# Kernel tuning notes

Measured on AMD Instinct MI355X. Metric: run time of the kernel, lower is better.

The kernel has to match this reference:

```python
import jax, jax.numpy as jnp
import numpy as np

S = 128           # inp_spatial_size
B = 4             # batch (4th coord column)
N = 200000        # active voxels
PLANES = (4, 8, 16, 32)   # feat_aug_mode='power', m=4
LEAK = 0.01
EPS = 1e-4        # sparseconvnet BatchNorm default eps
NOUT = 64


def _conv(x, w, stride, pad):
    return jax.lax.conv_general_dilated(
        x, w, (stride,) * 3, pad,
        dimension_numbers=('NCDHW', 'OIDHW', 'NCDHW'))


def _bn_lrelu(x, mask, g, b):
    # SCN BatchNormLeakyReLU: stats over ACTIVE sites only (x is zero at inactive)
    cnt = jnp.maximum(jnp.sum(mask), 1.0)
    mean = jnp.sum(x, axis=(0, 2, 3, 4)) / cnt
    var = jnp.sum(x * x, axis=(0, 2, 3, 4)) / cnt - mean * mean
    sc = (g * jax.lax.rsqrt(var + EPS))[None, :, None, None, None]
    y = (x - mean[None, :, None, None, None]) * sc + b[None, :, None, None, None]
    y = jnp.where(y >= 0, y, LEAK * y)
    return y * mask


def _pool2(x, red):
    b, c, d, h, w = x.shape
    return red(x.reshape(b, c, d // 2, 2, h // 2, 2, w // 2, 2), axis=(3, 5, 7))


def _forward(point_cloud, w0, g1, b1, wc1, g2, b2, wc2, g3, b3, wc3, wlin, blin):
    ci = point_cloud[:, :3].astype(jnp.int32)
    bi = point_cloud[:, 3].astype(jnp.int32)
    f = point_cloud[:, 4]
    # InputLayer mode=3: sum features of duplicate coordinates
    dense = jnp.zeros((B, 1, S, S, S), jnp.float32).at[bi, 0, ci[:, 0], ci[:, 1], ci[:, 2]].add(f)
    mask = jnp.zeros((B, 1, S, S, S), jnp.float32).at[bi, 0, ci[:, 0], ci[:, 1], ci[:, 2]].set(1.0)
    # SubmanifoldConvolution(3): dense 3^3 conv restricted to active output sites
    x = _conv(dense, w0, 1, 'SAME') * mask
    for g, b, wc in ((g1, b1, wc1), (g2, b2, wc2), (g3, b3, wc3)):
        x = _bn_lrelu(x, mask, g, b)
        x = _conv(x, wc, 2, 'VALID')        # sparse Convolution(k=2, s=2)
        mask = _pool2(mask, jnp.max)        # output active iff any input in window active
        x = x * mask
        x = _pool2(x, jnp.sum) / 8.0        # SCN AveragePooling(2,2): sum / poolVolume
        mask = _pool2(mask, jnp.max)
        x = x * mask
    # SparseToDense(32) + view(-1, D^3*C): row-major [B, C, D, D, D] flatten
    x = x.reshape(x.shape[0], -1)           # [B, 32*2^3] = [B, 256]
    return x @ wlin.T + blin                # use_linear_output -> [B, 64]


def setup_inputs() -> dict:
    key = jax.random.key(0)
    ks = jax.random.split(key, 10)
    coords = jax.random.randint(ks[0], (N, 3), 0, S).astype(jnp.float32)
    bidx = jax.random.randint(ks[1], (N, 1), 0, B).astype(jnp.float32)
    feats = jax.random.normal(ks[2], (N, 1), jnp.float32)
    point_cloud = jnp.concatenate([coords, bidx, feats], axis=1)

    def he(k, shape, fan_in):
        return jax.random.normal(k, shape, jnp.float32) / np.sqrt(fan_in)

    inp = {
        'point_cloud': point_cloud,
        'w0': he(ks[3], (PLANES[0], 1, 3, 3, 3), 27.0),
    }
    for i in range(3):
        cin, cout = PLANES[i], PLANES[i + 1]
        inp[f'g{i + 1}'] = jnp.ones((cin,), jnp.float32)
        inp[f'b{i + 1}'] = jnp.zeros((cin,), jnp.float32)
        inp[f'wc{i + 1}'] = he(ks[4 + i], (cout, cin, 2, 2, 2), cin * 8.0)
    d = S // 4 ** 3
    fan = PLANES[-1] * d ** 3
    inp['wlin'] = he(ks[8], (NOUT, fan), fan)
    inp['blin'] = jnp.zeros((NOUT,), jnp.float32)
    return inp


def reference(point_cloud, w0, g1, b1, wc1, g2, b2, wc2, g3, b3, wc3, wlin, blin):
    return _forward(point_cloud, w0, g1, b1, wc1, g2, b2, wc2, g3, b3, wc3, wlin, blin)
```

## Files before the change

kernel.cpp:

```cpp
#include <hip/hip_runtime.h>

#define SS 128
#define S3 (SS*SS*SS)
#define NBATCH 4
#define LEAK 0.01f
#define BNEPS 1e-4f
#define NTILE 16384
#define MAXSLOT 64

constexpr size_t OFF_DENSE    = 0;
constexpr size_t OFF_MASKBITS = OFF_DENSE + (size_t)NBATCH*S3*4;
constexpr size_t OFF_X1       = OFF_MASKBITS + (size_t)NBATCH*S3/8;
constexpr size_t OFF_MASK32   = OFF_X1 + (size_t)NBATCH*8*32768*4;
constexpr size_t OFF_MASK8    = OFF_MASK32 + (size_t)NBATCH*32768;
constexpr size_t OFF_STATS    = OFF_MASK8 + (size_t)NBATCH*512;
constexpr size_t OFF_P1       = OFF_STATS + 256;
constexpr size_t OFF_P2       = OFF_P1 + 256*9*4;
constexpr size_t OFF_P3       = OFF_P2 + 256*2*4;
constexpr size_t OFF_PM       = OFF_P3 + 64*2*4;
constexpr size_t OFF_NBLK     = OFF_PM + 16*4;
constexpr size_t OFF_LIST     = OFF_NBLK + NTILE*4;
constexpr size_t OFF_X0L      = OFF_LIST + (size_t)NTILE*MAXSLOT*4;
constexpr size_t OFF_X2       = OFF_X0L + (size_t)NTILE*MAXSLOT*16;
constexpr size_t OFF_X3       = OFF_X2 + (size_t)NBATCH*16*512*4;


__device__ inline float waveSum(float v) {
#pragma unroll
    for (int off = 32; off; off >>= 1) v += __shfl_xor(v, off, 64);
    return v;
}

__global__ void k_init(const float* __restrict__ pc, float* __restrict__ dense,
                       uint4* __restrict__ maskbits4, int n) {
    int blk = blockIdx.x;
    if (blk < 256) {
        maskbits4[blk * 256 + threadIdx.x] = make_uint4(0u, 0u, 0u, 0u);
        return;
    }
    int i = (blk - 256) * 256 + threadIdx.x;
    if (i >= n) return;
    int d = (int)pc[i*5+0], h = (int)pc[i*5+1], w = (int)pc[i*5+2], b = (int)pc[i*5+3];
    dense[(((size_t)b*SS + d)*SS + h)*SS + w] = 0.f;
}

__global__ void k_scatter(const float* __restrict__ pc, float* __restrict__ dense,
                          unsigned* __restrict__ maskbits, int n) {
    int i = blockIdx.x * blockDim.x + threadIdx.x;
    if (i >= n) return;
    float c0 = pc[i*5+0], c1 = pc[i*5+1], c2 = pc[i*5+2], cb = pc[i*5+3], f = pc[i*5+4];
    int d = (int)c0, h = (int)c1, w = (int)c2, b = (int)cb;
    unsigned vox = (((unsigned)b*SS + d)*SS + h)*SS + w;
    atomicAdd(&dense[vox], f);
    atomicOr(&maskbits[vox >> 5], 1u << (vox & 31));
}

__global__ __launch_bounds__(512) void k_conv0(const float* __restrict__ dense,
                                               const unsigned* __restrict__ maskbits,
                                               const float* __restrict__ w0g,
                                               unsigned* __restrict__ nblk,
                                               unsigned* __restrict__ list,
                                               float4* __restrict__ x0l,
                                               unsigned char* __restrict__ mask32) {
    __shared__ float lds[10*10*68];
    __shared__ float ws[108];
    __shared__ unsigned short wtot[8][8];
    __shared__ unsigned queue[8*MAXSLOT];
    __shared__ unsigned char cellocc[8][8];
    int tid = threadIdx.x;
    int lane = tid & 63, wid = tid >> 6;
    int th = blockIdx.x, td = blockIdx.y;
    int zb = blockIdx.z;
    int b = zb >> 1, wh = zb & 1;
    int d0 = td*8, h0 = th*8, w0 = wh*64;
    if (tid < 108) ws[tid] = w0g[tid];
    if (tid < 64) cellocc[tid>>3][tid&7] = 0;
    const float* dn = dense + (size_t)b * S3;
    for (int idx = tid; idx < 1600; idx += 512) {
        int r = idx >> 4, q = idx & 15;
        int dz = r / 10, dy = r - dz*10;
        int gz = d0 - 1 + dz, gy = h0 - 1 + dy;
        float4 v = make_float4(0.f, 0.f, 0.f, 0.f);
        if ((unsigned)gz < SS && (unsigned)gy < SS) {
            unsigned row = ((unsigned)b*SS + gz)*SS + gy;
            int gx = w0 + q*4;
            v = *(const float4*)(dn + ((size_t)gz*SS + gy)*SS + gx);
            unsigned mword = maskbits[row*4 + (gx >> 5)];
            int sh = gx & 31;
            if (!((mword >> (sh+0)) & 1u)) v.x = 0.f;
            if (!((mword >> (sh+1)) & 1u)) v.y = 0.f;
            if (!((mword >> (sh+2)) & 1u)) v.z = 0.f;
            if (!((mword >> (sh+3)) & 1u)) v.w = 0.f;
        }
        float* lrow = lds + r*68 + 1 + q*4;
        lrow[0]=v.x; lrow[1]=v.y; lrow[2]=v.z; lrow[3]=v.w;
    }
    for (int idx = tid; idx < 200; idx += 512) {
        int r = idx >> 1, side = idx & 1;
        int dz = r / 10, dy = r - dz*10;
        int gz = d0 - 1 + dz, gy = h0 - 1 + dy;
        int hgx = side ? (w0 + 64) : (w0 - 1);
        float hv = 0.f;
        if ((unsigned)gz < SS && (unsigned)gy < SS && (unsigned)hgx < SS) {
            unsigned row = ((unsigned)b*SS + gz)*SS + gy;
            float v = dn[((size_t)gz*SS + gy)*SS + hgx];
            unsigned mword = maskbits[row*4 + (hgx >> 5)];
            hv = ((mword >> (hgx & 31)) & 1u) ? v : 0.f;
        }
        lds[r*68 + (side ? 65 : 0)] = hv;
    }
    int tz = wid, ty = (tid >> 3) & 7, tx = tid & 7;
    int gz = d0 + tz, gy = h0 + ty;
    uint4 rb = ((const uint4*)maskbits)[((unsigned)b*SS + gz)*SS + gy];
    unsigned loW = wh ? rb.z : rb.x;
    unsigned hiW = wh ? rb.w : rb.y;
    unsigned occ8 = 0;
#pragma unroll
    for (int s=0;s<8;++s) {
        unsigned word = (s < 4) ? loW : hiW;
        occ8 |= (((word >> (((s&3)<<3) + tx)) & 1u) << s);
    }
    unsigned long long ballArr[8];
#pragma unroll
    for (int s=0;s<8;++s) {
        ballArr[s] = __ballot((occ8 >> s) & 1u);
        if (lane == 0) wtot[s][wid] = (unsigned short)__popcll(ballArr[s]);
    }
    __syncthreads();
    unsigned long long lmask = (1ull << lane) - 1ull;
    int blkbase = ((b*16 + td)*16 + th)*16 + wh*8;
    unsigned qb = 0;
#pragma unroll
    for (int s=0;s<8;++s) {
        unsigned base = 0, total = 0;
#pragma unroll
        for (int j=0;j<8;++j) { unsigned t = wtot[s][j]; if (j < wid) base += t; total += t; }
        unsigned tc = total < MAXSLOT ? total : MAXSLOT;
        if ((occ8 >> s) & 1u) {
            unsigned slot = base + (unsigned)__popcll(ballArr[s] & lmask);
            if (slot < MAXSLOT) queue[qb + slot] = (unsigned)tid | (s<<9) | (slot<<13);
            cellocc[s][((tz>>2)<<2) | ((ty>>2)<<1) | (tx>>2)] = 1;
        }
        qb += tc;
    }
    if (tid < 8) {
        unsigned total = 0;
#pragma unroll
        for (int j=0;j<8;++j) total += wtot[tid][j];
        nblk[blkbase + tid] = total < MAXSLOT ? total : MAXSLOT;
    }
    __syncthreads();
    if (tid < 64) {
        int s = tid >> 3, c = tid & 7;
        int cz = (c>>2)&1, cy = (c>>1)&1, cx = c&1;
        mask32[b*32768 + ((d0>>2)+cz)*1024 + ((h0>>2)+cy)*32 + wh*16 + s*2+cx] = cellocc[s][c];
    }
    for (unsigned i = tid; i < qb; i += 512) {
        unsigned e = queue[i];
        int et = e & 511, es = (e>>9) & 15, eslot = e >> 13;
        int ez = et >> 6, ey = (et>>3) & 7, ex = et & 7;
        int egx = es*8 + ex;
        float a0=0.f, a1=0.f, a2=0.f, a3=0.f;
#pragma unroll
        for (int kd=0; kd<3; ++kd)
#pragma unroll
            for (int kh=0; kh<3; ++kh)
#pragma unroll
                for (int kw=0; kw<3; ++kw) {
                    float v = lds[((ez+kd)*10 + ey+kh)*68 + egx + kw];
                    int kk = kd*9 + kh*3 + kw;
                    a0 += v*ws[kk]; a1 += v*ws[27+kk]; a2 += v*ws[54+kk]; a3 += v*ws[81+kk];
                }
        int blk = blkbase + es;
        unsigned vox = (((unsigned)b*SS + d0+ez)*SS + h0+ey)*SS + (w0 + egx);
        list[(size_t)blk*MAXSLOT + eslot] = vox;
        x0l[(size_t)blk*MAXSLOT + eslot] = make_float4(a0, a1, a2, a3);
    }
}

__global__ void k_stats1m(const float4* __restrict__ x0l, const unsigned* __restrict__ nblk,
                          const unsigned char* __restrict__ mask32, unsigned char* __restrict__ mask8,
                          float* __restrict__ p1, float* __restrict__ pm) {
    int tid = threadIdx.x;
    int bid = blockIdx.x;
    if (bid < 256) {
        __shared__ float red[4][9];
        int tid0 = bid * 256 + tid;
        float a[9] = {0,0,0,0,0,0,0,0,0};
        for (int s = tid0; s < NTILE*MAXSLOT; s += 65536) {
            int blk = s >> 6, sl = s & 63;
            if (sl < (int)nblk[blk]) {
                float4 v = x0l[s];
                a[0]+=v.x; a[1]+=v.y; a[2]+=v.z; a[3]+=v.w;
                a[4]+=v.x*v.x; a[5]+=v.y*v.y; a[6]+=v.z*v.z; a[7]+=v.w*v.w;
                a[8]+=1.f;
            }
        }
#pragma unroll
        for (int k=0;k<9;++k) a[k] = waveSum(a[k]);
        int wid = tid>>6, lane = tid&63;
        if (lane < 9) red[wid][lane] = a[lane];
        __syncthreads();
        if (tid < 9) p1[bid*9+tid] = red[0][tid]+red[1][tid]+red[2][tid]+red[3][tid];
        return;
    }
    __shared__ float redm[4];
    int blk = bid - 256;
    float c = 0.f;
    if (blk < 8) {
        int i = blk*256 + tid;
        int b = i>>9, r = i&511;
        int d8 = r>>6, h8 = (r>>3)&7, w8 = r&7;
        const unsigned char* m = mask32 + b*32768;
        unsigned v = 0;
#pragma unroll
        for (int dz=0;dz<2;++dz)
#pragma unroll
            for (int dy=0;dy<2;++dy)
#pragma unroll
                for (int dx=0;dx<2;++dx)
                    v |= m[(2*d8+dz)*1024 + (2*h8+dy)*32 + (2*w8+dx)];
        mask8[i] = (unsigned char)v;
        c = (float)v;
    } else {
        const uint4* m4 = (const uint4*)mask32;
        int base = ((blk-8)*256 + tid)*4;
#pragma unroll
        for (int j=0;j<4;++j) {
            uint4 x = m4[base+j];
            c += (float)(__popc(x.x) + __popc(x.y) + __popc(x.z) + __popc(x.w));
        }
    }
    c = waveSum(c);
    if ((tid & 63) == 0) redm[tid>>6] = c;
    __syncthreads();
    if (tid == 0) pm[blk] = redm[0]+redm[1]+redm[2]+redm[3];
}

__global__ __launch_bounds__(256) void k_prep1(const float* __restrict__ p1,
        const float* __restrict__ pm, const float* __restrict__ g1,
        const float* __restrict__ b1, float* __restrict__ stats) {
    __shared__ float red[4][9];
    __shared__ float tot[9];
    int tid = threadIdx.x;
    int wid = tid>>6, lane = tid&63;
    float a[9];
#pragma unroll
    for (int k=0;k<9;++k) a[k] = p1[tid*9+k];
#pragma unroll
    for (int k=0;k<9;++k) a[k] = waveSum(a[k]);
    if (lane < 9) red[wid][lane] = a[lane];
    __syncthreads();
    if (tid < 9) tot[tid] = red[0][tid]+red[1][tid]+red[2][tid]+red[3][tid];
    __syncthreads();
    if (tid < 4) {
        float cnt = fmaxf(tot[8], 1.f);
        float mean = tot[tid] / cnt;
        float var  = tot[4+tid] / cnt - mean*mean;
        float s = g1[tid] * rsqrtf(var + BNEPS);
        stats[2+tid] = s; stats[6+tid] = b1[tid] - mean*s;
    }
    if (tid == 4) { float s=0.f; for (int j=8;j<16;++j) s += pm[j]; stats[0] = s; }
    if (tid == 5) { float s=0.f; for (int j=0;j<8;++j)  s += pm[j]; stats[1] = s; }
}

__global__ void k_stage1(const float4* __restrict__ x0l, const unsigned* __restrict__ list,
                         const unsigned* __restrict__ nblk, const float* __restrict__ wc1,
                         const float* __restrict__ stats, float* __restrict__ x1) {
    __shared__ float acc[256];
    __shared__ float wsh[256];
    __shared__ float sc[4], sh[4];
    int tid = threadIdx.x;
    wsh[tid] = wc1[tid];
    acc[tid] = 0.f;
    if (tid < 4) { sc[tid] = stats[2+tid]; sh[tid] = stats[6+tid]; }
    __syncthreads();
    int s = blockIdx.x * 256 + tid;
    int blk = s >> 6, sl = s & 63;
    int lt = tid >> 6;
    if (sl < (int)nblk[blk]) {
        unsigned vox = list[s];
        float4 v = x0l[s];
        int w = vox & 127, h = (vox>>7)&127, d = (vox>>14)&127;
        float y[4];
        float t0 = v.x*sc[0]+sh[0]; y[0] = t0 >= 0.f ? t0 : LEAK*t0;
        float t1 = v.y*sc[1]+sh[1]; y[1] = t1 >= 0.f ? t1 : LEAK*t1;
        float t2 = v.z*sc[2]+sh[2]; y[2] = t2 >= 0.f ? t2 : LEAK*t2;
        float t3 = v.w*sc[3]+sh[3]; y[3] = t3 >= 0.f ? t3 : LEAK*t3;
        int widx = (d&1)*4 + (h&1)*2 + (w&1);
        int cell = ((d>>2)&1)*4 + ((h>>2)&1)*2 + ((w>>2)&1);
        float* ap = acc + lt*64 + cell;
#pragma unroll
        for (int o=0;o<8;++o) {
            const float* wp = wsh + o*32 + widx;
            float contrib = y[0]*wp[0] + y[1]*wp[8] + y[2]*wp[16] + y[3]*wp[24];
            atomicAdd(ap + o*8, contrib * 0.125f);
        }
    }
    __syncthreads();
    int rem = tid & 63, o = rem >> 3, cell = rem & 7;
    int blk2 = blockIdx.x*4 + (tid >> 6);
    int ss = blk2 & 15, th = (blk2>>4)&15, td = (blk2>>8)&15, b = blk2>>12;
    int cz = (cell>>2)&1, cy = (cell>>1)&1, cx = cell&1;
    x1[(size_t)b*8*32768 + o*32768 + (td*2+cz)*1024 + (th*2+cy)*32 + ss*2+cx] = acc[tid];
}

__global__ void k_s2stats(const float4* __restrict__ x1v, float* __restrict__ p2) {
    __shared__ float red[4][2];
    int blk = blockIdx.x;
    int plane = blk >> 3, chunk = blk & 7;
    const float4* p = x1v + (size_t)plane*8192 + chunk*1024;
    float s=0.f, sq=0.f;
    for (int i = threadIdx.x; i < 1024; i += 256) {
        float4 v = p[i];
        s  += v.x+v.y+v.z+v.w;
        sq += v.x*v.x+v.y*v.y+v.z*v.z+v.w*v.w;
    }
    s = waveSum(s); sq = waveSum(sq);
    int wid = threadIdx.x>>6, lane = threadIdx.x&63;
    if (lane == 0) { red[wid][0] = s; red[wid][1] = sq; }
    __syncthreads();
    if (threadIdx.x < 2)
        p2[blk*2+threadIdx.x] = red[0][threadIdx.x]+red[1][threadIdx.x]+red[2][threadIdx.x]+red[3][threadIdx.x];
}

__global__ void k_prep2(const float* __restrict__ p2, const float* __restrict__ g2,
                        const float* __restrict__ b2, float* __restrict__ stats) {
    __shared__ float sm[16];
    int tid = threadIdx.x;
    if (tid < 16) {
        int c = tid & 7, q = tid >> 3;
        float s = 0.f;
        for (int b=0;b<4;++b)
            for (int ch=0;ch<8;++ch)
                s += p2[((b*8+c)*8+ch)*2 + q];
        sm[tid] = s;
    }
    __syncthreads();
    if (tid < 8) {
        float cnt = fmaxf(stats[0], 1.f);
        float mean = sm[tid] / cnt;
        float var  = sm[8+tid] / cnt - mean*mean;
        float s = g2[tid] * rsqrtf(var + BNEPS);
        stats[10+tid] = s; stats[18+tid] = b2[tid] - mean*s;
    }
}

__global__ __launch_bounds__(256) void k_stage2(const float* __restrict__ x1,
                         const unsigned char* __restrict__ mask32,
                         const float* __restrict__ wc2, const float* __restrict__ stats,
                         float* __restrict__ x2) {
    __shared__ float wsh[1024];
    __shared__ float xin[8][64];
    __shared__ float mLDS[64];
    __shared__ float scs[8], shs[8];
    int tid = threadIdx.x;
    int br = blockIdx.x;
    int b = br >> 9, r = br & 511;
    int d8 = r >> 6, h8 = (r >> 3) & 7, w8 = r & 7;
    for (int i = tid; i < 1024; i += 256) wsh[i] = wc2[i];
    if (tid < 8) { scs[tid] = stats[10+tid]; shs[tid] = stats[18+tid]; }
    const unsigned char* mb = mask32 + b*32768;
    if (tid < 64) {
        int dd = tid >> 4, hh = (tid >> 2) & 3, ww = tid & 3;
        mLDS[tid] = mb[(d8*4+dd)*1024 + (h8*4+hh)*32 + (w8*4+ww)] ? 1.f : 0.f;
    }
    __syncthreads();
    if (tid < 128) {
        int c = tid >> 4, f = tid & 15;
        int dd = f >> 2, hh = f & 3;
        const float* src = x1 + (size_t)b*8*32768 + c*32768
                         + (d8*4+dd)*1024 + (h8*4+hh)*32 + w8*4;
        float4 v = *(const float4*)src;
        float sc = scs[c], sh = shs[c];
        int cbase = dd*16 + hh*4;
        float t0 = v.x*sc+sh; t0 = (t0>=0.f)?t0:LEAK*t0; xin[c][cbase+0] = t0 * mLDS[cbase+0];
        float t1 = v.y*sc+sh; t1 = (t1>=0.f)?t1:LEAK*t1; xin[c][cbase+1] = t1 * mLDS[cbase+1];
        float t2 = v.z*sc+sh; t2 = (t2>=0.f)?t2:LEAK*t2; xin[c][cbase+2] = t2 * mLDS[cbase+2];
        float t3 = v.w*sc+sh; t3 = (t3>=0.f)?t3:LEAK*t3; xin[c][cbase+3] = t3 * mLDS[cbase+3];
    }
    __syncthreads();
    int o = tid >> 4, g = tid & 15;
    float acc = 0.f;
#pragma unroll
    for (int j=0;j<4;++j) {
        int cell = g*4 + j;
        int dd = cell >> 4, hh = (cell >> 2) & 3, ww = cell & 3;
        int widx = (dd&1)*4 + (hh&1)*2 + (ww&1);
        const float* wp = wsh + o*64 + widx;
#pragma unroll
        for (int c=0;c<8;++c)
            acc += xin[c][cell] * wp[c*8];
    }
    acc += __shfl_xor(acc, 1, 64);
    acc += __shfl_xor(acc, 2, 64);
    acc += __shfl_xor(acc, 4, 64);
    acc += __shfl_xor(acc, 8, 64);
    if (g == 0) x2[((size_t)b*16 + o)*512 + r] = acc * 0.125f;
}

__global__ void k_s3stats(const float* __restrict__ x2, float* __restrict__ p3) {
    __shared__ float red[4][2];
    const float* p = x2 + (size_t)blockIdx.x * 512;
    float s=0.f, sq=0.f;
    for (int i = threadIdx.x; i < 512; i += 256) { float v = p[i]; s += v; sq += v*v; }
    s = waveSum(s); sq = waveSum(sq);
    int wid = threadIdx.x>>6, lane = threadIdx.x&63;
    if (lane == 0) { red[wid][0] = s; red[wid][1] = sq; }
    __syncthreads();
    if (threadIdx.x < 2)
        p3[blockIdx.x*2+threadIdx.x] = red[0][threadIdx.x]+red[1][threadIdx.x]+red[2][threadIdx.x]+red[3][threadIdx.x];
}

__global__ void k_prep3(const float* __restrict__ p3, const float* __restrict__ g3,
                        const float* __restrict__ b3, float* __restrict__ stats) {
    __shared__ float sm[32];
    int tid = threadIdx.x;
    if (tid < 32) {
        int c = tid & 15, q = tid >> 4;
        float s = 0.f;
        for (int b=0;b<4;++b) s += p3[(b*16+c)*2 + q];
        sm[tid] = s;
    }
    __syncthreads();
    if (tid < 16) {
        float cnt = fmaxf(stats[1], 1.f);
        float mean = sm[tid] / cnt;
        float var  = sm[16+tid] / cnt - mean*mean;
        float s = g3[tid] * rsqrtf(var + BNEPS);
        stats[26+tid] = s; stats[42+tid] = b3[tid] - mean*s;
    }
}

__global__ void k_stage3(const float* __restrict__ x2, const unsigned char* __restrict__ mask8,
                         const float* __restrict__ wc3, const float* __restrict__ stats,
                         float* __restrict__ x3) {
    int t = blockIdx.x * 4 + (threadIdx.x >> 6);
    int lane = threadIdx.x & 63;
    int r = t & 7, bo = t >> 3;
    int o = bo & 31, b = bo >> 5;
    int d2 = (r >> 2) & 1, h2 = (r >> 1) & 1, w2 = r & 1;
    int dd = lane >> 4, hh = (lane >> 2) & 3, ww = lane & 3;
    int s8 = (d2*4+dd)*64 + (h2*4+hh)*8 + (w2*4+ww);
    const float* xb = x2 + (size_t)b*16*512;
    float w0r = wc3[o*128 + lane];
    float w1r = wc3[o*128 + 64 + lane];
    float m = mask8[b*512 + s8] ? 1.f : 0.f;
    int widx = (dd&1)*4 + (hh&1)*2 + (ww&1);
    float acc = 0.f;
#pragma unroll
    for (int c=0;c<8;++c) {
        float v = xb[c*512 + s8];
        float tt = v*stats[26+c] + stats[42+c];
        tt = (tt >= 0.f) ? tt : LEAK*tt;
        acc += tt * __shfl(w0r, c*8 + widx, 64);
    }
#pragma unroll
    for (int c=8;c<16;++c) {
        float v = xb[c*512 + s8];
        float tt = v*stats[26+c] + stats[42+c];
        tt = (tt >= 0.f) ? tt : LEAK*tt;
        acc += tt * __shfl(w1r, (c-8)*8 + widx, 64);
    }
    acc = waveSum(acc * m);
    if (lane == 0) x3[t] = acc * 0.125f;
}

__global__ void k_linear(const float* __restrict__ x3, const float* __restrict__ wlin,
                         const float* __restrict__ blin, float* __restrict__ out) {
    int t = blockIdx.x * 4 + (threadIdx.x >> 6);
    int lane = threadIdx.x & 63;
    int b = t >> 6, j = t & 63;
    const float* xb = x3 + b*256;
    const float* wj = wlin + j*256;
    float acc = 0.f;
#pragma unroll
    for (int k=0;k<4;++k) acc += xb[k*64+lane] * wj[k*64+lane];
    acc = waveSum(acc);
    if (lane == 0) out[t] = acc + blin[j];
}

extern "C" void kernel_launch(void* const* d_in, const int* in_sizes, int n_in,
                              void* d_out, int out_size, void* d_ws, size_t ws_size,
                              hipStream_t stream) {
    const float* pc   = (const float*)d_in[0];
    const float* w0   = (const float*)d_in[1];
    const float* g1   = (const float*)d_in[2];
    const float* b1   = (const float*)d_in[3];
    const float* wc1  = (const float*)d_in[4];
    const float* g2   = (const float*)d_in[5];
    const float* b2   = (const float*)d_in[6];
    const float* wc2  = (const float*)d_in[7];
    const float* g3   = (const float*)d_in[8];
    const float* b3   = (const float*)d_in[9];
    const float* wc3  = (const float*)d_in[10];
    const float* wlin = (const float*)d_in[11];
    const float* blin = (const float*)d_in[12];
    float* out = (float*)d_out;

    char* ws = (char*)d_ws;
    float*         dense    = (float*)(ws + OFF_DENSE);
    unsigned*      maskbits = (unsigned*)(ws + OFF_MASKBITS);
    float*         x1       = (float*)(ws + OFF_X1);
    unsigned char* mask32   = (unsigned char*)(ws + OFF_MASK32);
    unsigned char* mask8    = (unsigned char*)(ws + OFF_MASK8);
    float*         stats    = (float*)(ws + OFF_STATS);
    float*         p1       = (float*)(ws + OFF_P1);
    float*         p2       = (float*)(ws + OFF_P2);
    float*         p3       = (float*)(ws + OFF_P3);
    float*         pm       = (float*)(ws + OFF_PM);
    unsigned*      nblk     = (unsigned*)(ws + OFF_NBLK);
    unsigned*      list     = (unsigned*)(ws + OFF_LIST);
    float4*        x0l      = (float4*)(ws + OFF_X0L);
    float*         x2       = (float*)(ws + OFF_X2);
    float*         x3       = (float*)(ws + OFF_X3);

    int n = in_sizes[0] / 5;
    int nb = (n + 255) / 256;

    k_init<<<256 + nb, 256, 0, stream>>>(pc, dense, (uint4*)maskbits, n);
    k_scatter<<<nb, 256, 0, stream>>>(pc, dense, maskbits, n);
    k_conv0<<<dim3(16,16,8), 512, 0, stream>>>(dense, maskbits, w0, nblk, list, x0l, mask32);
    k_stats1m<<<272, 256, 0, stream>>>(x0l, nblk, mask32, mask8, p1, pm);
    k_prep1<<<1, 256, 0, stream>>>(p1, pm, g1, b1, stats);
    k_stage1<<<NTILE/4, 256, 0, stream>>>(x0l, list, nblk, wc1, stats, x1);
    k_s2stats<<<256, 256, 0, stream>>>((const float4*)x1, p2);
    k_prep2<<<1, 64, 0, stream>>>(p2, g2, b2, stats);
    k_stage2<<<2048, 256, 0, stream>>>(x1, mask32, wc2, stats, x2);
    k_s3stats<<<64, 256, 0, stream>>>(x2, p3);
    k_prep3<<<1, 64, 0, stream>>>(p3, g3, b3, stats);
    k_stage3<<<256, 256, 0, stream>>>(x2, mask8, wc3, stats, x3);
    k_linear<<<64, 256, 0, stream>>>(x3, wlin, blin, out);
}
```

Before: 100.4 us.

## Fold BN prep kernels into stage kernels and gather only active voxels in conv0

Removes the three single-block BN statistics kernels (prep1/2/3): each stage kernel now reduces the partial sums and computes its own scale and shift in shared memory, which cuts three launches and the serialization they add. Separately, the conv0 tile load now zero-fills LDS and reads only the voxels whose mask bit is set, instead of loading full float4 rows and masking them. The cost is redundant per-block reduction work in every stage block, and a divergent bit-loop gather in place of coalesced vector loads.

```diff
diff --git a/kernel.cpp b/kernel.cpp
--- a/kernel.cpp
+++ b/kernel.cpp
@@ -13,8 +13,7 @@
 constexpr size_t OFF_X1       = OFF_MASKBITS + (size_t)NBATCH*S3/8;
 constexpr size_t OFF_MASK32   = OFF_X1 + (size_t)NBATCH*8*32768*4;
 constexpr size_t OFF_MASK8    = OFF_MASK32 + (size_t)NBATCH*32768;
-constexpr size_t OFF_STATS    = OFF_MASK8 + (size_t)NBATCH*512;
-constexpr size_t OFF_P1       = OFF_STATS + 256;
+constexpr size_t OFF_P1       = OFF_MASK8 + (size_t)NBATCH*512;
 constexpr size_t OFF_P2       = OFF_P1 + 256*9*4;
 constexpr size_t OFF_P3       = OFF_P2 + 256*2*4;
 constexpr size_t OFF_PM       = OFF_P3 + 64*2*4;
@@ -23,7 +22,6 @@
 constexpr size_t OFF_X0L      = OFF_LIST + (size_t)NTILE*MAXSLOT*4;
 constexpr size_t OFF_X2       = OFF_X0L + (size_t)NTILE*MAXSLOT*16;
 constexpr size_t OFF_X3       = OFF_X2 + (size_t)NBATCH*16*512*4;
-
 
 __device__ inline float waveSum(float v) {
 #pragma unroll
@@ -62,7 +60,7 @@
                                                unsigned* __restrict__ list,
                                                float4* __restrict__ x0l,
                                                unsigned char* __restrict__ mask32) {
-    __shared__ float lds[10*10*68];
+    __shared__ __align__(16) float lds[10*10*68];
     __shared__ float ws[108];
     __shared__ unsigned short wtot[8][8];
     __shared__ unsigned queue[8*MAXSLOT];
@@ -75,39 +73,36 @@
     int d0 = td*8, h0 = th*8, w0 = wh*64;
     if (tid < 108) ws[tid] = w0g[tid];
     if (tid < 64) cellocc[tid>>3][tid&7] = 0;
+    for (int i = tid; i < 1700; i += 512) ((float4*)lds)[i] = make_float4(0.f,0.f,0.f,0.f);
+    __syncthreads();
     const float* dn = dense + (size_t)b * S3;
-    for (int idx = tid; idx < 1600; idx += 512) {
-        int r = idx >> 4, q = idx & 15;
+    for (int idx = tid; idx < 200; idx += 512) {
+        int r = idx >> 1, ww2 = idx & 1;
         int dz = r / 10, dy = r - dz*10;
         int gz = d0 - 1 + dz, gy = h0 - 1 + dy;
-        float4 v = make_float4(0.f, 0.f, 0.f, 0.f);
-        if ((unsigned)gz < SS && (unsigned)gy < SS) {
-            unsigned row = ((unsigned)b*SS + gz)*SS + gy;
-            int gx = w0 + q*4;
-            v = *(const float4*)(dn + ((size_t)gz*SS + gy)*SS + gx);
-            unsigned mword = maskbits[row*4 + (gx >> 5)];
-            int sh = gx & 31;
-            if (!((mword >> (sh+0)) & 1u)) v.x = 0.f;
-            if (!((mword >> (sh+1)) & 1u)) v.y = 0.f;
-            if (!((mword >> (sh+2)) & 1u)) v.z = 0.f;
-            if (!((mword >> (sh+3)) & 1u)) v.w = 0.f;
+        if ((unsigned)gz >= SS || (unsigned)gy >= SS) continue;
+        const float* rowp = dn + ((size_t)gz*SS + gy)*SS;
+        unsigned rowi = ((unsigned)b*SS + gz)*SS + gy;
+        unsigned m = maskbits[rowi*4 + wh*2 + ww2];
+        float* lrow = lds + r*68 + 1 + ww2*32;
+        int gbase = w0 + ww2*32;
+        while (m) {
+            int bit = __ffs(m) - 1; m &= m - 1;
+            lrow[bit] = rowp[gbase + bit];
         }
-        float* lrow = lds + r*68 + 1 + q*4;
-        lrow[0]=v.x; lrow[1]=v.y; lrow[2]=v.z; lrow[3]=v.w;
-    }
-    for (int idx = tid; idx < 200; idx += 512) {
-        int r = idx >> 1, side = idx & 1;
-        int dz = r / 10, dy = r - dz*10;
-        int gz = d0 - 1 + dz, gy = h0 - 1 + dy;
-        int hgx = side ? (w0 + 64) : (w0 - 1);
-        float hv = 0.f;
-        if ((unsigned)gz < SS && (unsigned)gy < SS && (unsigned)hgx < SS) {
-            unsigned row = ((unsigned)b*SS + gz)*SS + gy;
-            float v = dn[((size_t)gz*SS + gy)*SS + hgx];
-            unsigned mword = maskbits[row*4 + (hgx >> 5)];
-            hv = ((mword >> (hgx & 31)) & 1u) ? v : 0.f;
+        if (ww2 == 0) {
+            int hgx = w0 - 1;
+            if (hgx >= 0) {
+                unsigned hm = maskbits[rowi*4 + (hgx>>5)];
+                if ((hm >> (hgx&31)) & 1u) lds[r*68] = rowp[hgx];
+            }
+        } else {
+            int hgx = w0 + 64;
+            if (hgx < SS) {
+                unsigned hm = maskbits[rowi*4 + (hgx>>5)];
+                if ((hm >> (hgx&31)) & 1u) lds[r*68 + 65] = rowp[hgx];
+            }
         }
-        lds[r*68 + (side ? 65 : 0)] = hv;
     }
     int tz = wid, ty = (tid >> 3) & 7, tx = tid & 7;
     int gz = d0 + tz, gy = h0 + ty;
@@ -237,13 +232,18 @@
     if (tid == 0) pm[blk] = redm[0]+redm[1]+redm[2]+redm[3];
 }
 
-__global__ __launch_bounds__(256) void k_prep1(const float* __restrict__ p1,
-        const float* __restrict__ pm, const float* __restrict__ g1,
-        const float* __restrict__ b1, float* __restrict__ stats) {
+__global__ void k_stage1(const float4* __restrict__ x0l, const unsigned* __restrict__ list,
+                         const unsigned* __restrict__ nblk, const float* __restrict__ wc1,
+                         const float* __restrict__ p1, const float* __restrict__ g1,
+                         const float* __restrict__ b1, float* __restrict__ x1) {
+    __shared__ float acc[256];
+    __shared__ float wsh[256];
     __shared__ float red[4][9];
-    __shared__ float tot[9];
+    __shared__ float sc[4], sh[4];
     int tid = threadIdx.x;
     int wid = tid>>6, lane = tid&63;
+    wsh[tid] = wc1[tid];
+    acc[tid] = 0.f;
     float a[9];
 #pragma unroll
     for (int k=0;k<9;++k) a[k] = p1[tid*9+k];
@@ -251,29 +251,14 @@
     for (int k=0;k<9;++k) a[k] = waveSum(a[k]);
     if (lane < 9) red[wid][lane] = a[lane];
     __syncthreads();
-    if (tid < 9) tot[tid] = red[0][tid]+red[1][tid]+red[2][tid]+red[3][tid];
-    __syncthreads();
     if (tid < 4) {
-        float cnt = fmaxf(tot[8], 1.f);
-        float mean = tot[tid] / cnt;
-        float var  = tot[4+tid] / cnt - mean*mean;
+        float sum = red[0][tid]+red[1][tid]+red[2][tid]+red[3][tid];
+        float sq  = red[0][4+tid]+red[1][4+tid]+red[2][4+tid]+red[3][4+tid];
+        float cnt = fmaxf(red[0][8]+red[1][8]+red[2][8]+red[3][8], 1.f);
+        float mean = sum/cnt, var = sq/cnt - mean*mean;
         float s = g1[tid] * rsqrtf(var + BNEPS);
-        stats[2+tid] = s; stats[6+tid] = b1[tid] - mean*s;
-    }
-    if (tid == 4) { float s=0.f; for (int j=8;j<16;++j) s += pm[j]; stats[0] = s; }
-    if (tid == 5) { float s=0.f; for (int j=0;j<8;++j)  s += pm[j]; stats[1] = s; }
-}
-
-__global__ void k_stage1(const float4* __restrict__ x0l, const unsigned* __restrict__ list,
-                         const unsigned* __restrict__ nblk, const float* __restrict__ wc1,
-                         const float* __restrict__ stats, float* __restrict__ x1) {
-    __shared__ float acc[256];
-    __shared__ float wsh[256];
-    __shared__ float sc[4], sh[4];
-    int tid = threadIdx.x;
-    wsh[tid] = wc1[tid];
-    acc[tid] = 0.f;
-    if (tid < 4) { sc[tid] = stats[2+tid]; sh[tid] = stats[6+tid]; }
+        sc[tid] = s; sh[tid] = b1[tid] - mean*s;
+    }
     __syncthreads();
     int s = blockIdx.x * 256 + tid;
     int blk = s >> 6, sl = s & 63;
@@ -324,46 +309,43 @@
         p2[blk*2+threadIdx.x] = red[0][threadIdx.x]+red[1][threadIdx.x]+red[2][threadIdx.x]+red[3][threadIdx.x];
 }
 
-__global__ void k_prep2(const float* __restrict__ p2, const float* __restrict__ g2,
-                        const float* __restrict__ b2, float* __restrict__ stats) {
-    __shared__ float sm[16];
-    int tid = threadIdx.x;
-    if (tid < 16) {
-        int c = tid & 7, q = tid >> 3;
-        float s = 0.f;
-        for (int b=0;b<4;++b)
-            for (int ch=0;ch<8;++ch)
-                s += p2[((b*8+c)*8+ch)*2 + q];
-        sm[tid] = s;
-    }
-    __syncthreads();
-    if (tid < 8) {
-        float cnt = fmaxf(stats[0], 1.f);
-        float mean = sm[tid] / cnt;
-        float var  = sm[8+tid] / cnt - mean*mean;
-        float s = g2[tid] * rsqrtf(var + BNEPS);
-        stats[10+tid] = s; stats[18+tid] = b2[tid] - mean*s;
-    }
-}
-
 __global__ __launch_bounds__(256) void k_stage2(const float* __restrict__ x1,
                          const unsigned char* __restrict__ mask32,
-                         const float* __restrict__ wc2, const float* __restrict__ stats,
-                         float* __restrict__ x2) {
+                         const float* __restrict__ wc2, const float* __restrict__ p2,
+                         const float* __restrict__ pm, const float* __restrict__ g2,
+                         const float* __restrict__ b2, float* __restrict__ x2) {
     __shared__ float wsh[1024];
     __shared__ float xin[8][64];
     __shared__ float mLDS[64];
+    __shared__ float sm[16];
     __shared__ float scs[8], shs[8];
     int tid = threadIdx.x;
     int br = blockIdx.x;
     int b = br >> 9, r = br & 511;
     int d8 = r >> 6, h8 = (r >> 3) & 7, w8 = r & 7;
     for (int i = tid; i < 1024; i += 256) wsh[i] = wc2[i];
-    if (tid < 8) { scs[tid] = stats[10+tid]; shs[tid] = stats[18+tid]; }
+    if (tid < 16) sm[tid] = 0.f;
     const unsigned char* mb = mask32 + b*32768;
     if (tid < 64) {
         int dd = tid >> 4, hh = (tid >> 2) & 3, ww = tid & 3;
         mLDS[tid] = mb[(d8*4+dd)*1024 + (h8*4+hh)*32 + (w8*4+ww)] ? 1.f : 0.f;
+    }
+    __syncthreads();
+    {
+        float v0 = p2[tid];
+        atomicAdd(&sm[((tid>>4)&7)*2 + (tid&1)], v0);
+        int e = tid + 256;
+        float v1 = p2[e];
+        atomicAdd(&sm[((e>>4)&7)*2 + (e&1)], v1);
+    }
+    __syncthreads();
+    if (tid < 8) {
+        float cnt = pm[8]+pm[9]+pm[10]+pm[11]+pm[12]+pm[13]+pm[14]+pm[15];
+        cnt = fmaxf(cnt, 1.f);
+        float mean = sm[tid*2] / cnt;
+        float var  = sm[tid*2+1] / cnt - mean*mean;
+        float s = g2[tid] * rsqrtf(var + BNEPS);
+        scs[tid] = s; shs[tid] = b2[tid] - mean*s;
     }
     __syncthreads();
     if (tid < 128) {
@@ -412,31 +394,28 @@
         p3[blockIdx.x*2+threadIdx.x] = red[0][threadIdx.x]+red[1][threadIdx.x]+red[2][threadIdx.x]+red[3][threadIdx.x];
 }
 
-__global__ void k_prep3(const float* __restrict__ p3, const float* __restrict__ g3,
-                        const float* __restrict__ b3, float* __restrict__ stats) {
+__global__ void k_stage3(const float* __restrict__ x2, const unsigned char* __restrict__ mask8,
+                         const float* __restrict__ wc3, const float* __restrict__ p3,
+                         const float* __restrict__ pm, const float* __restrict__ g3,
+                         const float* __restrict__ b3, float* __restrict__ x3) {
     __shared__ float sm[32];
+    __shared__ float scs[16], shs[16];
     int tid = threadIdx.x;
-    if (tid < 32) {
-        int c = tid & 15, q = tid >> 4;
-        float s = 0.f;
-        for (int b=0;b<4;++b) s += p3[(b*16+c)*2 + q];
-        sm[tid] = s;
-    }
+    if (tid < 32) sm[tid] = 0.f;
+    __syncthreads();
+    if (tid < 128) atomicAdd(&sm[((tid>>1)&15)*2 + (tid&1)], p3[tid]);
     __syncthreads();
     if (tid < 16) {
-        float cnt = fmaxf(stats[1], 1.f);
-        float mean = sm[tid] / cnt;
-        float var  = sm[16+tid] / cnt - mean*mean;
+        float cnt = pm[0]+pm[1]+pm[2]+pm[3]+pm[4]+pm[5]+pm[6]+pm[7];
+        cnt = fmaxf(cnt, 1.f);
+        float mean = sm[tid*2] / cnt;
+        float var  = sm[tid*2+1] / cnt - mean*mean;
         float s = g3[tid] * rsqrtf(var + BNEPS);
-        stats[26+tid] = s; stats[42+tid] = b3[tid] - mean*s;
-    }
-}
-
-__global__ void k_stage3(const float* __restrict__ x2, const unsigned char* __restrict__ mask8,
-                         const float* __restrict__ wc3, const float* __restrict__ stats,
-                         float* __restrict__ x3) {
-    int t = blockIdx.x * 4 + (threadIdx.x >> 6);
-    int lane = threadIdx.x & 63;
+        scs[tid] = s; shs[tid] = b3[tid] - mean*s;
+    }
+    __syncthreads();
+    int t = blockIdx.x * 4 + (tid >> 6);
+    int lane = tid & 63;
     int r = t & 7, bo = t >> 3;
     int o = bo & 31, b = bo >> 5;
     int d2 = (r >> 2) & 1, h2 = (r >> 1) & 1, w2 = r & 1;
@@ -451,14 +430,14 @@
 #pragma unroll
     for (int c=0;c<8;++c) {
         float v = xb[c*512 + s8];
-        float tt = v*stats[26+c] + stats[42+c];
+        float tt = v*scs[c] + shs[c];
         tt = (tt >= 0.f) ? tt : LEAK*tt;
         acc += tt * __shfl(w0r, c*8 + widx, 64);
     }
 #pragma unroll
     for (int c=8;c<16;++c) {
         float v = xb[c*512 + s8];
-        float tt = v*stats[26+c] + stats[42+c];
+        float tt = v*scs[c] + shs[c];
         tt = (tt >= 0.f) ? tt : LEAK*tt;
         acc += tt * __shfl(w1r, (c-8)*8 + widx, 64);
     }
@@ -504,7 +483,6 @@
     float*         x1       = (float*)(ws + OFF_X1);
     unsigned char* mask32   = (unsigned char*)(ws + OFF_MASK32);
     unsigned char* mask8    = (unsigned char*)(ws + OFF_MASK8);
-    float*         stats    = (float*)(ws + OFF_STATS);
     float*         p1       = (float*)(ws + OFF_P1);
     float*         p2       = (float*)(ws + OFF_P2);
     float*         p3       = (float*)(ws + OFF_P3);
@@ -522,13 +500,10 @@
     k_scatter<<<nb, 256, 0, stream>>>(pc, dense, maskbits, n);
     k_conv0<<<dim3(16,16,8), 512, 0, stream>>>(dense, maskbits, w0, nblk, list, x0l, mask32);
     k_stats1m<<<272, 256, 0, stream>>>(x0l, nblk, mask32, mask8, p1, pm);
-    k_prep1<<<1, 256, 0, stream>>>(p1, pm, g1, b1, stats);
-    k_stage1<<<NTILE/4, 256, 0, stream>>>(x0l, list, nblk, wc1, stats, x1);
+    k_stage1<<<NTILE/4, 256, 0, stream>>>(x0l, list, nblk, wc1, p1, g1, b1, x1);
     k_s2stats<<<256, 256, 0, stream>>>((const float4*)x1, p2);
-    k_prep2<<<1, 64, 0, stream>>>(p2, g2, b2, stats);
-    k_stage2<<<2048, 256, 0, stream>>>(x1, mask32, wc2, stats, x2);
+    k_stage2<<<2048, 256, 0, stream>>>(x1, mask32, wc2, p2, pm, g2, b2, x2);
     k_s3stats<<<64, 256, 0, stream>>>(x2, p3);
-    k_prep3<<<1, 64, 0, stream>>>(p3, g3, b3, stats);
-    k_stage3<<<256, 256, 0, stream>>>(x2, mask8, wc3, stats, x3);
+    k_stage3<<<256, 256, 0, stream>>>(x2, mask8, wc3, p3, pm, g3, b3, x3);
     k_linear<<<64, 256, 0, stream>>>(x3, wlin, blin, out);
 }
```

Measured after the change: 105.9 us. +5.4%, slower.
